# Optimization experiments

Hardware: AMD Instinct MI355X
Metric: run time of the kernel (lower is better)

Reference implementation:

```python
import jax, jax.numpy as jnp
import numpy as np

B, N = 128, 1024            # batch, sample_count
MIN_S, MAX_S, STEP = 4.0, 104.0, 1.0  # scale range -> S = 101 scales
OUT_H, OUT_W = 200, 200     # output_size


def morlet_kernels():
    # scales = tf.range(min_scale, max_scale+1, step)
    scales = jnp.arange(MIN_S, MAX_S + 1.0, STEP, dtype=jnp.float32)  # (S,)
    t = jnp.arange(N, dtype=jnp.float32) - (N - 1.0) / 2.0            # centered time
    times = t[None, :] / scales[:, None]                               # (S, N)
    return jnp.exp(-0.5 * times ** 2) * jnp.cos(5.0 * times)          # morlet


def setup_inputs() -> dict:
    key = jax.random.key(0)
    x = jax.random.normal(key, (B, N), dtype=jnp.float32)
    kernels = morlet_kernels()  # (S, N), non-trainable param built in build()
    return {"x": x, "kernels": kernels}


def reference(x, kernels):
    # x: (B, N) signals; kernels: (S, N) scaled wavelets.
    # Original per-sample op: conv1d(kernels[S,N,1], filter=reverse(x)[N,1,1], SAME)
    # -> correlation of each wavelet row with the reversed signal (= convolution with x).
    n = x.shape[1]
    pad_l = (n - 1) // 2           # TF 'SAME' padding, stride 1, filter length n
    pad_r = (n - 1) - pad_l
    x_rev = x[:, ::-1]
    # One grouped conv: lhs=(S,1,N) NCW, rhs=(B,1,N) OIW -> out (S,B,N)
    res = jax.lax.conv_general_dilated(
        kernels[:, None, :], x_rev[:, None, :],
        window_strides=(1,), padding=[(pad_l, pad_r)],
        dimension_numbers=("NCW", "OIW", "NCW"))
    res = jnp.transpose(res, (1, 0, 2))  # (B, S, N)
    # global (per-sample) min-max normalization
    mn = jnp.min(res, axis=(1, 2), keepdims=True)
    mx = jnp.max(res, axis=(1, 2), keepdims=True)
    res_norm = (res - mn) / (mx - mn)
    img = res_norm[..., None]  # (B, S, N, 1)
    # tf.image.resize default: bilinear, antialias=False, half-pixel centers
    out = jax.image.resize(img, (img.shape[0], OUT_H, OUT_W, 1),
                           method="bilinear", antialias=False)
    return out
```

## Files before the change

kernel.cpp:

```cpp
#include <hip/hip_runtime.h>
#include <hip/hip_bf16.h>

#define NB 128
#define NS 101
#define NW 1024
#define OH 200
#define OW 200
#define EPS 1034

typedef __bf16 bf16x8 __attribute__((ext_vector_type(8)));
typedef float f32x4 __attribute__((ext_vector_type(4)));

__device__ __forceinline__ void gload_lds16(const void* gsrc, void* ldst) {
    __builtin_amdgcn_global_load_lds(
        (const __attribute__((address_space(1))) void*)gsrc,
        (__attribute__((address_space(3))) void*)ldst, 16, 0, 0);
}

__device__ __forceinline__ unsigned encf(float f) {
    unsigned u = __float_as_uint(f);
    return (u & 0x80000000u) ? ~u : (u | 0x80000000u);
}
__device__ __forceinline__ float decf(unsigned e) {
    unsigned u = (e & 0x80000000u) ? (e ^ 0x80000000u) : ~e;
    return __uint_as_float(u);
}

__global__ __launch_bounds__(256) void prep_kernel(const float* __restrict__ K,
                                                   ushort* __restrict__ Kbf,
                                                   unsigned* __restrict__ mm) {
    int blk = blockIdx.x;
    if (blk < 112) {
        int c = threadIdx.x * 4;
        float4 v = make_float4(0.f, 0.f, 0.f, 0.f);
        if (blk < NS) v = *(const float4*)(K + (size_t)blk * NW + c);
        ushort4 o;
        __hip_bfloat16 h;
        h = __float2bfloat16(v.x); o.x = reinterpret_cast<const ushort&>(h);
        h = __float2bfloat16(v.y); o.y = reinterpret_cast<const ushort&>(h);
        h = __float2bfloat16(v.z); o.z = reinterpret_cast<const ushort&>(h);
        h = __float2bfloat16(v.w); o.w = reinterpret_cast<const ushort&>(h);
        *(ushort4*)(Kbf + (size_t)blk * NW + c) = o;
    } else {
        int t = threadIdx.x;
        mm[t] = (t < NB) ? 0xFFFFFFFFu : 0u;
    }
}


#define STAGE_T(t, lo, hi, base)                                              \
    _Pragma("unroll")                                                         \
    for (int s = (lo); s <= (hi); ++s) {                                      \
        if ((((base) + s - (lo)) & 7) == wv)                                  \
            gload_lds16(Kbf + (size_t)(16 * (t) + n) * NW + 32 * s + 8 * g,   \
                        &A_lds[((base) + s - (lo)) * 512]);                   \
    }

#define MFMA_T(t, lo, hi, base, ti)                                           \
    if (s >= (lo) && s <= (hi)) {                                             \
        bf16x8 af = *(const bf16x8*)&A_lds[((base) + s - (lo)) * 512 + lane * 8]; \
        _Pragma("unroll")                                                     \
        for (int nt = 0; nt < 8; ++nt)                                        \
            acc[ti][nt] = __builtin_amdgcn_mfma_f32_16x16x32_bf16(            \
                af, ring[(2 * s - nt) & 7], acc[ti][nt], 0, 0, 0);            \
    }

#define EPI_T(t, ti)                                                          \
    {                                                                         \
        _Pragma("unroll")                                                     \
        for (int nt = 0; nt < 8; ++nt) {                                      \
            _Pragma("unroll")                                                 \
            for (int r = 0; r < 4; ++r) {                                     \
                const int row16 = 4 * g + r;                                  \
                float v = acc[ti][nt][r];                                     \
                if (16 * (t) + row16 < NS) { mn = fminf(mn, v); mx = fmaxf(mx, v); } \
                epi[row16 * EPS + wbase + 16 * nt + n] = v;                   \
            }                                                                 \
        }                                                                     \
        __syncthreads();                                                      \
        for (int idx = tid; idx < 16 * OW; idx += 512) {                      \
            const int row16 = idx / OW;                                       \
            const int j = idx % OW;                                           \
            const int srow = 16 * (t) + row16;                                \
            if (srow < NS) {                                                  \
                const float xx = (j + 0.5f) * (1024.0f / 200.0f) - 0.5f;      \
                const float xf = floorf(xx);                                  \
                const float fx = xx - xf;                                     \
                int j0 = (int)xf, j1 = j0 + 1;                                \
                j0 = max(0, min(NW - 1, j0)); j1 = max(0, min(NW - 1, j1));   \
                tmp[((size_t)b * NS + srow) * OW + j] =                       \
                    (1.f - fx) * epi[row16 * EPS + j0] + fx * epi[row16 * EPS + j1]; \
            }                                                                 \
        }                                                                     \
        __syncthreads();                                                      \
    }

__global__ __launch_bounds__(512, 1) void conv_mfma(
        const float* __restrict__ x, const ushort* __restrict__ Kbf,
        float* __restrict__ tmp, unsigned* __restrict__ mm) {
    __shared__ __align__(16) char smem[118912];
    ushort* A_lds = (ushort*)smem;
    ushort* xSh = (ushort*)(smem + 86016);
    float* epi = (float*)smem;

    const int tid = threadIdx.x;
    const int bid = blockIdx.x;
    const int cls = bid >> 7;
    const int b = bid & 127;
    const int wv = tid >> 6;
    const int lane = tid & 63;
    const int n = lane & 15;
    const int g = lane >> 4;

    {
        const float* xb = x + (size_t)b * NW;
        for (int idx = tid; idx < 8 * 257; idx += 512) {
            int dlt = idx / 257;
            int i0 = (idx % 257) * 8;
            union { ushort us[8]; uint4 v; } pk;
            #pragma unroll
            for (int j = 0; j < 8; ++j) {
                int ir = i0 + j + dlt;
                float f = (ir >= 512 && ir < 1536) ? xb[1535 - ir] : 0.0f;
                __hip_bfloat16 h = __float2bfloat16(f);
                pk.us[j] = reinterpret_cast<const ushort&>(h);
            }
            *reinterpret_cast<uint4*>(&xSh[dlt * 2056 + i0]) = pk.v;
        }
    }

    if (cls == 0) {
        STAGE_T(0, 12, 19, 0)
        STAGE_T(1,  9, 22, 8)
        STAGE_T(3,  3, 28, 22)
        STAGE_T(4,  0, 31, 48)
    } else {
        STAGE_T(2,  6, 25, 0)
        STAGE_T(5,  0, 31, 20)
        STAGE_T(6,  0, 31, 52)
    }
    __syncthreads();

    const int dlt = (7 - n) & 7;
    const int wbase = wv * 128;
    const ushort* bp = xSh + dlt * 2056 + (1023 - wbase - n + 8 * g - dlt);

    float mn = 3.4e38f, mx = -3.4e38f;

    if (cls == 0) {
        f32x4 acc[4][8];
        #pragma unroll
        for (int ti = 0; ti < 4; ++ti)
            #pragma unroll
            for (int nt = 0; nt < 8; ++nt)
                acc[ti][nt] = (f32x4){0.f, 0.f, 0.f, 0.f};
        bf16x8 ring[8];
        #pragma unroll
        for (int f = -7; f <= 0; ++f)
            ring[f & 7] = *(const bf16x8*)(bp + 16 * f);
        #pragma unroll
        for (int s = 0; s < 32; ++s) {
            if (s > 0) {
                ring[(2 * s - 1) & 7] = *(const bf16x8*)(bp + 16 * (2 * s - 1));
                ring[(2 * s) & 7]     = *(const bf16x8*)(bp + 16 * (2 * s));
            }
            MFMA_T(0, 12, 19, 0, 0)
            MFMA_T(1,  9, 22, 8, 1)
            MFMA_T(3,  3, 28, 22, 2)
            MFMA_T(4,  0, 31, 48, 3)
        }
        __syncthreads();
        EPI_T(0, 0)
        EPI_T(1, 1)
        EPI_T(3, 2)
        EPI_T(4, 3)
    } else {
        f32x4 acc[3][8];
        #pragma unroll
        for (int ti = 0; ti < 3; ++ti)
            #pragma unroll
            for (int nt = 0; nt < 8; ++nt)
                acc[ti][nt] = (f32x4){0.f, 0.f, 0.f, 0.f};
        bf16x8 ring[8];
        #pragma unroll
        for (int f = -7; f <= 0; ++f)
            ring[f & 7] = *(const bf16x8*)(bp + 16 * f);
        #pragma unroll
        for (int s = 0; s < 32; ++s) {
            if (s > 0) {
                ring[(2 * s - 1) & 7] = *(const bf16x8*)(bp + 16 * (2 * s - 1));
                ring[(2 * s) & 7]     = *(const bf16x8*)(bp + 16 * (2 * s));
            }
            MFMA_T(2,  6, 25, 0, 0)
            MFMA_T(5,  0, 31, 20, 1)
            MFMA_T(6,  0, 31, 52, 2)
        }
        __syncthreads();
        EPI_T(2, 0)
        EPI_T(5, 1)
        EPI_T(6, 2)
    }

    #pragma unroll
    for (int off = 32; off > 0; off >>= 1) {
        mn = fminf(mn, __shfl_down(mn, off));
        mx = fmaxf(mx, __shfl_down(mx, off));
    }
    if (lane == 0) {
        atomicMin(&mm[b], encf(mn));
        atomicMax(&mm[NB + b], encf(mx));
    }
}

__global__ __launch_bounds__(256) void resize_v(
        const float* __restrict__ tmp, const unsigned* __restrict__ mm,
        float* __restrict__ out) {
    int idx = blockIdx.x * 256 + threadIdx.x;
    if (idx >= NB * OH * OW) return;
    const int j = idx % OW;
    const int i = (idx / OW) % OH;
    const int b = idx / (OW * OH);
    const float mn = decf(mm[b]);
    const float inv = 1.0f / (decf(mm[NB + b]) - mn);
    const float y = (i + 0.5f) * (101.0f / 200.0f) - 0.5f;
    const float yf = floorf(y);
    const float fy = y - yf;
    int i0 = (int)yf, i1 = i0 + 1;
    i0 = max(0, min(NS - 1, i0)); i1 = max(0, min(NS - 1, i1));
    const float* tp = tmp + (size_t)b * NS * OW;
    float v = (1.f - fy) * tp[i0 * OW + j] + fy * tp[i1 * OW + j];
    out[idx] = (v - mn) * inv;
}

extern "C" void kernel_launch(void* const* d_in, const int* in_sizes, int n_in,
                              void* d_out, int out_size, void* d_ws, size_t ws_size,
                              hipStream_t stream) {
    const float* x = (const float*)d_in[0];
    const float* K = (const float*)d_in[1];
    float* out = (float*)d_out;

    char* ws = (char*)d_ws;
    unsigned* mm = (unsigned*)ws;
    ushort* Kbf = (ushort*)(ws + 1024);
    float* tmp = (float*)(ws + 1024 + (size_t)112 * NW * 2);

    hipLaunchKernelGGL(prep_kernel, dim3(113), dim3(256), 0, stream, K, Kbf, mm);
    hipLaunchKernelGGL(conv_mfma, dim3(256), dim3(512), 0, stream, x, Kbf, tmp, mm);
    const int t2 = NB * OH * OW;
    hipLaunchKernelGGL(resize_v, dim3((t2 + 255) / 256), dim3(256), 0, stream, tmp, mm, out);
}
```

Measured before the change: 103.6 us.

## Fuse kernel bf16 conversion into conv, drop atomics, store intermediate in bf16

Removes the prep kernel: the conv kernel now reads fp32 wavelet rows directly, converts them to bf16 in registers and writes them to LDS, replacing the async global-to-LDS loads. Per-sample min/max are reduced within the block and written to distinct slots per class, which removes the atomics and the initialisation step. The resize kernel merges the two class slots. The horizontally resized intermediate is stored as bf16 to halve its traffic, at the cost of extra precision loss and of synchronous staging loads in the conv loop.

```diff
diff --git a/kernel.cpp b/kernel.cpp
--- a/kernel.cpp
+++ b/kernel.cpp
@@ -11,49 +11,30 @@
 typedef __bf16 bf16x8 __attribute__((ext_vector_type(8)));
 typedef float f32x4 __attribute__((ext_vector_type(4)));
 
-__device__ __forceinline__ void gload_lds16(const void* gsrc, void* ldst) {
-    __builtin_amdgcn_global_load_lds(
-        (const __attribute__((address_space(1))) void*)gsrc,
-        (__attribute__((address_space(3))) void*)ldst, 16, 0, 0);
-}
-
-__device__ __forceinline__ unsigned encf(float f) {
-    unsigned u = __float_as_uint(f);
-    return (u & 0x80000000u) ? ~u : (u | 0x80000000u);
-}
-__device__ __forceinline__ float decf(unsigned e) {
-    unsigned u = (e & 0x80000000u) ? (e ^ 0x80000000u) : ~e;
-    return __uint_as_float(u);
-}
-
-__global__ __launch_bounds__(256) void prep_kernel(const float* __restrict__ K,
-                                                   ushort* __restrict__ Kbf,
-                                                   unsigned* __restrict__ mm) {
-    int blk = blockIdx.x;
-    if (blk < 112) {
-        int c = threadIdx.x * 4;
-        float4 v = make_float4(0.f, 0.f, 0.f, 0.f);
-        if (blk < NS) v = *(const float4*)(K + (size_t)blk * NW + c);
-        ushort4 o;
-        __hip_bfloat16 h;
-        h = __float2bfloat16(v.x); o.x = reinterpret_cast<const ushort&>(h);
-        h = __float2bfloat16(v.y); o.y = reinterpret_cast<const ushort&>(h);
-        h = __float2bfloat16(v.z); o.z = reinterpret_cast<const ushort&>(h);
-        h = __float2bfloat16(v.w); o.w = reinterpret_cast<const ushort&>(h);
-        *(ushort4*)(Kbf + (size_t)blk * NW + c) = o;
-    } else {
-        int t = threadIdx.x;
-        mm[t] = (t < NB) ? 0xFFFFFFFFu : 0u;
-    }
-}
-
 
 #define STAGE_T(t, lo, hi, base)                                              \
     _Pragma("unroll")                                                         \
     for (int s = (lo); s <= (hi); ++s) {                                      \
-        if ((((base) + s - (lo)) & 7) == wv)                                  \
-            gload_lds16(Kbf + (size_t)(16 * (t) + n) * NW + 32 * s + 8 * g,   \
-                        &A_lds[((base) + s - (lo)) * 512]);                   \
+        if ((((base) + s - (lo)) & 7) == wv) {                                \
+            const int row = 16 * (t) + n;                                     \
+            union { ushort us[8]; uint4 v; } pk;                              \
+            pk.v = (uint4){0u, 0u, 0u, 0u};                                   \
+            if (row < NS) {                                                   \
+                const float* kp = K + (size_t)row * NW + 32 * s + 8 * g;      \
+                const float4 f0 = *(const float4*)kp;                         \
+                const float4 f1 = *(const float4*)(kp + 4);                   \
+                __hip_bfloat16 h;                                             \
+                h = __float2bfloat16(f0.x); pk.us[0] = reinterpret_cast<const ushort&>(h); \
+                h = __float2bfloat16(f0.y); pk.us[1] = reinterpret_cast<const ushort&>(h); \
+                h = __float2bfloat16(f0.z); pk.us[2] = reinterpret_cast<const ushort&>(h); \
+                h = __float2bfloat16(f0.w); pk.us[3] = reinterpret_cast<const ushort&>(h); \
+                h = __float2bfloat16(f1.x); pk.us[4] = reinterpret_cast<const ushort&>(h); \
+                h = __float2bfloat16(f1.y); pk.us[5] = reinterpret_cast<const ushort&>(h); \
+                h = __float2bfloat16(f1.z); pk.us[6] = reinterpret_cast<const ushort&>(h); \
+                h = __float2bfloat16(f1.w); pk.us[7] = reinterpret_cast<const ushort&>(h); \
+            }                                                                 \
+            *(uint4*)&A_lds[((base) + s - (lo)) * 512 + lane * 8] = pk.v;     \
+        }                                                                     \
     }
 
 #define MFMA_T(t, lo, hi, base, ti)                                           \
@@ -88,20 +69,21 @@
                 const float fx = xx - xf;                                     \
                 int j0 = (int)xf, j1 = j0 + 1;                                \
                 j0 = max(0, min(NW - 1, j0)); j1 = max(0, min(NW - 1, j1));   \
-                tmp[((size_t)b * NS + srow) * OW + j] =                       \
-                    (1.f - fx) * epi[row16 * EPS + j0] + fx * epi[row16 * EPS + j1]; \
+                tmp[((size_t)b * NS + srow) * OW + j] = __float2bfloat16(     \
+                    (1.f - fx) * epi[row16 * EPS + j0] + fx * epi[row16 * EPS + j1]); \
             }                                                                 \
         }                                                                     \
         __syncthreads();                                                      \
     }
 
 __global__ __launch_bounds__(512, 1) void conv_mfma(
-        const float* __restrict__ x, const ushort* __restrict__ Kbf,
-        float* __restrict__ tmp, unsigned* __restrict__ mm) {
+        const float* __restrict__ x, const float* __restrict__ K,
+        __hip_bfloat16* __restrict__ tmp, float* __restrict__ mm) {
     __shared__ __align__(16) char smem[118912];
     ushort* A_lds = (ushort*)smem;
     ushort* xSh = (ushort*)(smem + 86016);
     float* epi = (float*)smem;
+    __shared__ float smn[8], smx[8];
 
     const int tid = threadIdx.x;
     const int bid = blockIdx.x;
@@ -206,29 +188,39 @@
         mn = fminf(mn, __shfl_down(mn, off));
         mx = fmaxf(mx, __shfl_down(mx, off));
     }
-    if (lane == 0) {
-        atomicMin(&mm[b], encf(mn));
-        atomicMax(&mm[NB + b], encf(mx));
+    if (lane == 0) { smn[wv] = mn; smx[wv] = mx; }
+    __syncthreads();
+    if (tid == 0) {
+        float bmn = smn[0], bmx = smx[0];
+        #pragma unroll
+        for (int w = 1; w < 8; ++w) {
+            bmn = fminf(bmn, smn[w]);
+            bmx = fmaxf(bmx, smx[w]);
+        }
+        mm[cls * 256 + b] = bmn;
+        mm[cls * 256 + 128 + b] = bmx;
     }
 }
 
 __global__ __launch_bounds__(256) void resize_v(
-        const float* __restrict__ tmp, const unsigned* __restrict__ mm,
+        const __hip_bfloat16* __restrict__ tmp, const float* __restrict__ mm,
         float* __restrict__ out) {
     int idx = blockIdx.x * 256 + threadIdx.x;
     if (idx >= NB * OH * OW) return;
     const int j = idx % OW;
     const int i = (idx / OW) % OH;
     const int b = idx / (OW * OH);
-    const float mn = decf(mm[b]);
-    const float inv = 1.0f / (decf(mm[NB + b]) - mn);
+    const float mn = fminf(mm[b], mm[256 + b]);
+    const float mx = fmaxf(mm[128 + b], mm[384 + b]);
+    const float inv = 1.0f / (mx - mn);
     const float y = (i + 0.5f) * (101.0f / 200.0f) - 0.5f;
     const float yf = floorf(y);
     const float fy = y - yf;
     int i0 = (int)yf, i1 = i0 + 1;
     i0 = max(0, min(NS - 1, i0)); i1 = max(0, min(NS - 1, i1));
-    const float* tp = tmp + (size_t)b * NS * OW;
-    float v = (1.f - fy) * tp[i0 * OW + j] + fy * tp[i1 * OW + j];
+    const __hip_bfloat16* tp = tmp + (size_t)b * NS * OW;
+    float v = (1.f - fy) * __bfloat162float(tp[i0 * OW + j])
+            + fy * __bfloat162float(tp[i1 * OW + j]);
     out[idx] = (v - mn) * inv;
 }
 
@@ -240,12 +232,10 @@
     float* out = (float*)d_out;
 
     char* ws = (char*)d_ws;
-    unsigned* mm = (unsigned*)ws;
-    ushort* Kbf = (ushort*)(ws + 1024);
-    float* tmp = (float*)(ws + 1024 + (size_t)112 * NW * 2);
-
-    hipLaunchKernelGGL(prep_kernel, dim3(113), dim3(256), 0, stream, K, Kbf, mm);
-    hipLaunchKernelGGL(conv_mfma, dim3(256), dim3(512), 0, stream, x, Kbf, tmp, mm);
+    float* mm = (float*)ws;
+    __hip_bfloat16* tmp = (__hip_bfloat16*)(ws + 4096);
+
+    hipLaunchKernelGGL(conv_mfma, dim3(256), dim3(512), 0, stream, x, K, tmp, mm);
     const int t2 = NB * OH * OW;
     hipLaunchKernelGGL(resize_v, dim3((t2 + 255) / 256), dim3(256), 0, stream, tmp, mm, out);
 }
```

After: 99.55 us. 1.04x faster.
